# Optimization experiments

Measured on AMD Instinct MI355X. Metric: run time of the kernel, lower is better.

## Reference

```python
import jax, jax.numpy as jnp
import numpy as np

N_NODES = 100000
N_EDGES = 1600000


def setup_inputs() -> dict:
    key = jax.random.key(0)
    ks = jax.random.split(key, 8)
    x = jax.random.normal(ks[0], (N_NODES, 100), dtype=jnp.float32)
    edge_index = jax.random.randint(ks[1], (2, N_EDGES), 0, N_NODES, dtype=jnp.int64)
    edge_weight = jax.random.uniform(ks[2], (N_EDGES,), dtype=jnp.float32)
    # params (kaiming-ish scale)
    W_conv = jax.random.normal(ks[3], (100, 32), dtype=jnp.float32) * (1.0 / np.sqrt(100))
    b_conv = jnp.zeros((32,), jnp.float32)
    W1 = jax.random.normal(ks[4], (32, 16), dtype=jnp.float32) * (1.0 / np.sqrt(32))
    b1 = jnp.zeros((16,), jnp.float32)
    W2 = jax.random.normal(ks[5], (16, 8), dtype=jnp.float32) * (1.0 / np.sqrt(16))
    b2 = jnp.zeros((8,), jnp.float32)
    W3 = jax.random.normal(ks[6], (8, 10), dtype=jnp.float32) * (1.0 / np.sqrt(8))
    b3 = jnp.zeros((10,), jnp.float32)
    return {"x": x, "edge_index": edge_index, "edge_weight": edge_weight,
            "W_conv": W_conv, "b_conv": b_conv, "W1": W1, "b1": b1,
            "W2": W2, "b2": b2, "W3": W3, "b3": b3}


def gcn_conv(x, edge_index, W, b, n_nodes):
    # PyG GCNConv: add self-loops, symmetric deg^-0.5 normalization, unit edge weights
    loop = jnp.arange(n_nodes, dtype=edge_index.dtype)
    src = jnp.concatenate([edge_index[0], loop])
    dst = jnp.concatenate([edge_index[1], loop])
    deg = jax.ops.segment_sum(jnp.ones_like(dst, dtype=x.dtype), dst,
                              num_segments=n_nodes)
    dinv = jax.lax.rsqrt(jnp.maximum(deg, 1e-12))  # deg >= 1 due to self-loops
    norm = dinv[src] * dinv[dst]                   # [E+N]
    h = x @ W                                      # [N, 32]
    msg = h[src] * norm[:, None]                   # gather + scale
    out = jax.ops.segment_sum(msg, dst, num_segments=n_nodes)  # scatter-add
    return out + b


def reference(x, edge_index, edge_weight, W_conv, b_conv, W1, b1, W2, b2, W3, b3):
    # edge_weight is accepted by the original forward but never used (conv1(x, edge_index))
    n_nodes = x.shape[0]
    h = jax.nn.relu(gcn_conv(x, edge_index, W_conv, b_conv, n_nodes))
    # F.dropout with training=False (eval) is identity
    h = jax.nn.relu(h @ W1 + b1)
    h = jax.nn.relu(h @ W2 + b2)
    h = h @ W3 + b3
    return jax.nn.log_softmax(h, axis=1)
```

## Files before the change

### kernel.cpp

```cpp
#include <hip/hip_runtime.h>
#include <hip/hip_fp16.h>
#include <math.h>

#define N_NODES 100000
#define N_EDGES 1600000
#define F_IN 100
#define F_H 32

#define BKT_SHIFT 7
#define BKT_C 128
#define NBK 782
#define BKT_CAP 2560
#define BF_B 1024
#define BF_EPT 8
#define BF_TILE 8192
#define BF_GRID 196
#define AG_B 512
#define AG_CAP BKT_CAP
#define AG_EPT 5

#define XW_B 256
#define XW_R 128
#define XW_S2 51

__global__ __launch_bounds__(BF_B) void binfill_kernel(
        const int* __restrict__ src, const int* __restrict__ dst,
        int* __restrict__ gcursor, unsigned* __restrict__ packed) {
    __shared__ int cnt[NBK];
    __shared__ int lbase[NBK];
    __shared__ int gbase[NBK];
    __shared__ int wsums[16];
    __shared__ unsigned stage[BF_TILE];
    __shared__ unsigned short stageB[BF_TILE];
    __shared__ int tot;
    int t = threadIdx.x;
    long base = (long)blockIdx.x * BF_TILE;
    for (int i = t; i < NBK; i += BF_B) cnt[i] = 0;
    __syncthreads();
    int myb[BF_EPT]; int mypos[BF_EPT]; unsigned mypk[BF_EPT];
#pragma unroll
    for (int k = 0; k < BF_EPT; k++) {
        long e = base + t + (long)k * BF_B;
        myb[k] = -1;
        if (e < N_EDGES) {
            int d = dst[e];
            int sI = src[e];
            int b = d >> BKT_SHIFT;
            myb[k] = b;
            mypk[k] = (unsigned)sI | ((unsigned)(d & (BKT_C - 1)) << 17);
            mypos[k] = atomicAdd(&cnt[b], 1);
        }
    }
    __syncthreads();
    if (t < NBK && cnt[t] > 0)
        gbase[t] = t * BKT_CAP + atomicAdd(&gcursor[t], cnt[t]);
    int lane = t & 63, w = t >> 6;
    int v = (t < NBK) ? cnt[t] : 0;
    int sc = v;
#pragma unroll
    for (int off = 1; off < 64; off <<= 1) {
        int x = __shfl_up(sc, off, 64);
        if (lane >= off) sc += x;
    }
    if (lane == 63) wsums[w] = sc;
    __syncthreads();
    int pre = 0;
#pragma unroll
    for (int u = 0; u < 16; u++) pre += (u < w) ? wsums[u] : 0;
    int incl = sc + pre;
    if (t < NBK) lbase[t] = incl - v;
    if (t == BF_B - 1) tot = incl;
    __syncthreads();
#pragma unroll
    for (int k = 0; k < BF_EPT; k++) {
        if (myb[k] >= 0) {
            int p = lbase[myb[k]] + mypos[k];
            stage[p] = mypk[k];
            stageB[p] = (unsigned short)myb[k];
        }
    }
    __syncthreads();
    int T = tot;
    for (int i = t; i < T; i += BF_B) {
        int b = stageB[i];
        packed[gbase[b] + (i - lbase[b])] = stage[i];
    }
}

__global__ __launch_bounds__(XW_B) void degxw_kernel(
        const int* __restrict__ blen, const unsigned* __restrict__ packed,
        const float* __restrict__ x, const float* __restrict__ W,
        float* __restrict__ dinv, __half* __restrict__ h2) {
    __shared__ __half2 xs[XW_R * XW_S2];
    __shared__ int cnt[BKT_C];
    __shared__ float sdinv[BKT_C];
    int t = threadIdx.x;
    int b = blockIdx.x;
    if (t < BKT_C) cnt[t] = 0;
    __syncthreads();
    int beg = b * BKT_CAP, end = beg + blen[b];
    for (int i = beg + t; i < end; i += XW_B)
        atomicAdd(&cnt[(packed[i] >> 17) & (BKT_C - 1)], 1);
    __syncthreads();
    int rbase = b << BKT_SHIFT;
    int rows = min(XW_R, N_NODES - rbase);
    if (t < BKT_C) {
        float dv = rsqrtf((float)cnt[t] + 1.0f);
        sdinv[t] = dv;
        if (t < rows) dinv[rbase + t] = dv;
    }
    int total = rows * F_IN;
    const float4* gx4 = (const float4*)(x + (long)rbase * F_IN);
    for (int i4 = t; i4 < (total >> 2); i4 += XW_B) {
        float4 v = gx4[i4];
        int i = i4 << 2;
        int r = i / F_IN;
        int k = i - r * F_IN;
        __half2* p = xs + r * XW_S2 + (k >> 1);
        p[0] = __floats2half2_rn(v.x, v.y);
        p[1] = __floats2half2_rn(v.z, v.w);
    }
    __syncthreads();
    int r = t & (XW_R - 1);
    int colh16 = __builtin_amdgcn_readfirstlane((t >> 7) << 4);
    if (r < rows) {
        const float* Wp = W + colh16;
        float acc[16];
#pragma unroll
        for (int j = 0; j < 16; j++) acc[j] = 0.f;
        const __half2* xr = xs + r * XW_S2;
#pragma unroll 5
        for (int k2 = 0; k2 < F_IN / 2; k2++) {
            float2 xv = __half22float2(xr[k2]);
#pragma unroll
            for (int j = 0; j < 16; j++)
                acc[j] = fmaf(xv.y, Wp[(2 * k2 + 1) * F_H + j],
                              fmaf(xv.x, Wp[(2 * k2) * F_H + j], acc[j]));
        }
        float dv = sdinv[r];
        __half2 o[8];
#pragma unroll
        for (int j = 0; j < 8; j++)
            o[j] = __halves2half2(__float2half(acc[2 * j] * dv),
                                  __float2half(acc[2 * j + 1] * dv));
        float4* dst4 = (float4*)(h2 + (long)(rbase + r) * F_H + colh16);
        dst4[0] = ((float4*)o)[0];
        dst4[1] = ((float4*)o)[1];
    }
}

__global__ __launch_bounds__(AG_B) void agg_kernel(
        const int* __restrict__ blen, const unsigned* __restrict__ packed,
        const __half* __restrict__ h2, const float* __restrict__ dinv,
        const float* __restrict__ bc,
        const float* __restrict__ W1, const float* __restrict__ b1,
        const float* __restrict__ W2, const float* __restrict__ b2,
        const float* __restrict__ W3, const float* __restrict__ b3,
        float* __restrict__ out) {
    __shared__ float accL[BKT_C * 33];
    __shared__ int esrc[AG_CAP];
    __shared__ int cnt[BKT_C];
    __shared__ int lbase[BKT_C];
    __shared__ int wsum;
    __shared__ float sbc[32], sW1[512], sb1[16], sW2[128], sb2[8], sW3[80], sb3[10];
    int t = threadIdx.x;
    if (t < 32) sbc[t] = bc[t];
    if (t < 512) sW1[t] = W1[t];
    if (t < 16) sb1[t] = b1[t];
    if (t < 128) sW2[t] = W2[t];
    if (t < 8) sb2[t] = b2[t];
    if (t < 80) sW3[t] = W3[t];
    if (t < 10) sb3[t] = b3[t];

    int b = blockIdx.x;
    int beg = b * BKT_CAP;
    int cnum = blen[b];
    if (t < BKT_C) cnt[t] = 0;
    __syncthreads();
    unsigned pk[AG_EPT]; int pos[AG_EPT];
#pragma unroll
    for (int k = 0; k < AG_EPT; k++) {
        int idx = t + k * AG_B;
        pk[k] = 0xFFFFFFFFu;
        if (idx < cnum) {
            unsigned p = packed[beg + idx];
            pk[k] = p;
            pos[k] = atomicAdd(&cnt[(p >> 17) & (BKT_C - 1)], 1);
        }
    }
    __syncthreads();
    {
        int lane = t & 63;
        int v = 0;
        if (t < BKT_C) {
            v = cnt[t];
#pragma unroll
            for (int off = 1; off < 64; off <<= 1) {
                int xx = __shfl_up(v, off, 64);
                if (lane >= off) v += xx;
            }
            if (t == 63) wsum = v;
        }
        __syncthreads();
        if (t < BKT_C) {
            if (t >= 64) v += wsum;
            lbase[t] = v;
        }
    }
    __syncthreads();
#pragma unroll
    for (int k = 0; k < AG_EPT; k++) {
        if (pk[k] != 0xFFFFFFFFu) {
            int lid = (pk[k] >> 17) & (BKT_C - 1);
            esrc[lbase[lid] - cnt[lid] + pos[k]] = (int)(pk[k] & 0x1FFFF);
        }
    }
    __syncthreads();
    {
        int g = t >> 2, l = t & 3;
        const float4* h2o = (const float4*)h2;
        int e = lbase[g] - cnt[g];
        int eend = lbase[g];
        float a0 = 0.f, a1 = 0.f, a2 = 0.f, a3 = 0.f;
        float a4 = 0.f, a5 = 0.f, a6 = 0.f, a7 = 0.f;
        for (; e + 8 <= eend; e += 8) {
            int s0 = esrc[e], s1 = esrc[e+1], s2 = esrc[e+2], s3 = esrc[e+3];
            int s4 = esrc[e+4], s5 = esrc[e+5], s6 = esrc[e+6], s7 = esrc[e+7];
            float4 q0 = h2o[s0 * 4 + l];
            float4 q1 = h2o[s1 * 4 + l];
            float4 q2 = h2o[s2 * 4 + l];
            float4 q3 = h2o[s3 * 4 + l];
            float4 q4 = h2o[s4 * 4 + l];
            float4 q5 = h2o[s5 * 4 + l];
            float4 q6 = h2o[s6 * 4 + l];
            float4 q7 = h2o[s7 * 4 + l];
#pragma unroll
            for (int u = 0; u < 8; u++) {
                float4 q = (u == 0) ? q0 : (u == 1) ? q1 : (u == 2) ? q2 :
                           (u == 3) ? q3 : (u == 4) ? q4 : (u == 5) ? q5 :
                           (u == 6) ? q6 : q7;
                const __half2* hp = (const __half2*)&q;
                float2 f0 = __half22float2(hp[0]);
                float2 f1 = __half22float2(hp[1]);
                float2 f2 = __half22float2(hp[2]);
                float2 f3 = __half22float2(hp[3]);
                a0 += f0.x; a1 += f0.y; a2 += f1.x; a3 += f1.y;
                a4 += f2.x; a5 += f2.y; a6 += f3.x; a7 += f3.y;
            }
        }
        for (; e < eend; e++) {
            float4 q = h2o[esrc[e] * 4 + l];
            const __half2* hp = (const __half2*)&q;
            float2 f0 = __half22float2(hp[0]);
            float2 f1 = __half22float2(hp[1]);
            float2 f2 = __half22float2(hp[2]);
            float2 f3 = __half22float2(hp[3]);
            a0 += f0.x; a1 += f0.y; a2 += f1.x; a3 += f1.y;
            a4 += f2.x; a5 += f2.y; a6 += f3.x; a7 += f3.y;
        }
        float* ap = accL + g * 33 + 8 * l;
        ap[0] = a0; ap[1] = a1; ap[2] = a2; ap[3] = a3;
        ap[4] = a4; ap[5] = a5; ap[6] = a6; ap[7] = a7;
    }
    __syncthreads();

    int n = (b << BKT_SHIFT) + t;
    if (t < BKT_C && n < N_NODES) {
        float dv = dinv[n];
        const __half2* h2v = (const __half2*)h2;
        float a[32];
#pragma unroll
        for (int q = 0; q < 16; q++) {
            float2 hv = __half22float2(h2v[n * 16 + q]);
            a[2*q]   = fmaxf((accL[t * 33 + 2*q]   + hv.x) * dv + sbc[2*q],   0.f);
            a[2*q+1] = fmaxf((accL[t * 33 + 2*q+1] + hv.y) * dv + sbc[2*q+1], 0.f);
        }
        float t1[16];
#pragma unroll
        for (int j = 0; j < 16; j++) {
            float s = sb1[j];
            for (int k = 0; k < 32; k++) s += a[k] * sW1[k * 16 + j];
            t1[j] = fmaxf(s, 0.f);
        }
        float t2[8];
#pragma unroll
        for (int j = 0; j < 8; j++) {
            float s = sb2[j];
            for (int k = 0; k < 16; k++) s += t1[k] * sW2[k * 8 + j];
            t2[j] = fmaxf(s, 0.f);
        }
        float t3[10];
#pragma unroll
        for (int j = 0; j < 10; j++) {
            float s = sb3[j];
            for (int k = 0; k < 8; k++) s += t2[k] * sW3[k * 10 + j];
            t3[j] = s;
        }
        float m = t3[0];
#pragma unroll
        for (int j = 1; j < 10; j++) m = fmaxf(m, t3[j]);
        float se = 0.f;
#pragma unroll
        for (int j = 0; j < 10; j++) se += expf(t3[j] - m);
        float lse = logf(se) + m;
        float* op = out + (long)n * 10;
#pragma unroll
        for (int j = 0; j < 10; j++) op[j] = t3[j] - lse;
    }
}

extern "C" void kernel_launch(void* const* d_in, const int* in_sizes, int n_in,
                              void* d_out, int out_size, void* d_ws, size_t ws_size,
                              hipStream_t stream) {
    const float* x  = (const float*)d_in[0];
    const int*   ei = (const int*)d_in[1];
    const float* Wc = (const float*)d_in[3];
    const float* bc = (const float*)d_in[4];
    const float* W1 = (const float*)d_in[5];
    const float* b1 = (const float*)d_in[6];
    const float* W2 = (const float*)d_in[7];
    const float* b2 = (const float*)d_in[8];
    const float* W3 = (const float*)d_in[9];
    const float* b3 = (const float*)d_in[10];
    float* out = (float*)d_out;

    __half*   h2      = (__half*)d_ws;
    unsigned* packed  = (unsigned*)((char*)d_ws + (long)N_NODES * F_H * 2);
    float*    dinv    = (float*)(packed + (long)NBK * BKT_CAP);
    int*      gcursor = (int*)(dinv + N_NODES);

    const int* srcp = ei;
    const int* dstp = ei + N_EDGES;

    hipMemsetAsync(gcursor, 0, NBK * sizeof(int), stream);
    binfill_kernel<<<BF_GRID, BF_B, 0, stream>>>(srcp, dstp, gcursor, packed);
    degxw_kernel<<<NBK, XW_B, 0, stream>>>(gcursor, packed, x, Wc, dinv, h2);
    agg_kernel<<<NBK, AG_B, 0, stream>>>(gcursor, packed, h2, dinv, bc, W1, b1, W2, b2,
                                         W3, b3, out);
}
```

Before: 173.4 us.

## Split each aggregation bucket across two half-blocks of 64 destination nodes

The aggregation kernel now launches two 256-thread blocks per 128-node bucket. Each block reads the whole bucket's packed edge list but keeps only the edges whose destination falls in its half, then bins, gathers and runs the MLP for 64 nodes. This doubles the grid, cuts shared memory per block and turns the two-wavefront scan into a single-wavefront scan, aiming for higher occupancy and more parallelism. In exchange every packed edge is read twice, and each thread now holds 9 edge slots, which raises register pressure.

```diff
diff --git a/kernel.cpp b/kernel.cpp
--- a/kernel.cpp
+++ b/kernel.cpp
@@ -15,9 +15,9 @@
 #define BF_EPT 8
 #define BF_TILE 8192
 #define BF_GRID 196
-#define AG_B 512
-#define AG_CAP BKT_CAP
-#define AG_EPT 5
+#define AG_B 256
+#define AG_EPT 9
+#define AG_HCAP 1280
 
 #define XW_B 256
 #define XW_R 128
@@ -157,25 +157,25 @@
         const float* __restrict__ W2, const float* __restrict__ b2,
         const float* __restrict__ W3, const float* __restrict__ b3,
         float* __restrict__ out) {
-    __shared__ float accL[BKT_C * 33];
-    __shared__ int esrc[AG_CAP];
-    __shared__ int cnt[BKT_C];
-    __shared__ int lbase[BKT_C];
-    __shared__ int wsum;
+    __shared__ float accL[64 * 33];
+    __shared__ int esrc[AG_HCAP];
+    __shared__ int cnt[64];
+    __shared__ int lbase[64];
     __shared__ float sbc[32], sW1[512], sb1[16], sW2[128], sb2[8], sW3[80], sb3[10];
     int t = threadIdx.x;
     if (t < 32) sbc[t] = bc[t];
-    if (t < 512) sW1[t] = W1[t];
+    for (int i = t; i < 512; i += AG_B) sW1[i] = W1[i];
     if (t < 16) sb1[t] = b1[t];
     if (t < 128) sW2[t] = W2[t];
     if (t < 8) sb2[t] = b2[t];
     if (t < 80) sW3[t] = W3[t];
     if (t < 10) sb3[t] = b3[t];
 
-    int b = blockIdx.x;
-    int beg = b * BKT_CAP;
-    int cnum = blen[b];
-    if (t < BKT_C) cnt[t] = 0;
+    int bb = blockIdx.x >> 1;
+    int hh = blockIdx.x & 1;
+    int beg = bb * BKT_CAP;
+    int cnum = blen[bb];
+    if (t < 64) cnt[t] = 0;
     __syncthreads();
     unsigned pk[AG_EPT]; int pos[AG_EPT];
 #pragma unroll
@@ -184,35 +184,30 @@
         pk[k] = 0xFFFFFFFFu;
         if (idx < cnum) {
             unsigned p = packed[beg + idx];
-            pk[k] = p;
-            pos[k] = atomicAdd(&cnt[(p >> 17) & (BKT_C - 1)], 1);
-        }
-    }
-    __syncthreads();
-    {
-        int lane = t & 63;
-        int v = 0;
-        if (t < BKT_C) {
-            v = cnt[t];
-#pragma unroll
-            for (int off = 1; off < 64; off <<= 1) {
-                int xx = __shfl_up(v, off, 64);
-                if (lane >= off) v += xx;
+            int lid7 = (p >> 17) & (BKT_C - 1);
+            if ((lid7 >> 6) == hh) {
+                pk[k] = p;
+                pos[k] = atomicAdd(&cnt[lid7 & 63], 1);
             }
-            if (t == 63) wsum = v;
-        }
-        __syncthreads();
-        if (t < BKT_C) {
-            if (t >= 64) v += wsum;
-            lbase[t] = v;
-        }
+        }
+    }
+    __syncthreads();
+    if (t < 64) {
+        int v = cnt[t];
+        int sc = v;
+#pragma unroll
+        for (int off = 1; off < 64; off <<= 1) {
+            int xx = __shfl_up(sc, off, 64);
+            if ((t & 63) >= off) sc += xx;
+        }
+        lbase[t] = sc;
     }
     __syncthreads();
 #pragma unroll
     for (int k = 0; k < AG_EPT; k++) {
         if (pk[k] != 0xFFFFFFFFu) {
-            int lid = (pk[k] >> 17) & (BKT_C - 1);
-            esrc[lbase[lid] - cnt[lid] + pos[k]] = (int)(pk[k] & 0x1FFFF);
+            int g = (pk[k] >> 17) & 63;
+            esrc[lbase[g] - cnt[g] + pos[k]] = (int)(pk[k] & 0x1FFFF);
         }
     }
     __syncthreads();
@@ -264,8 +259,8 @@
     }
     __syncthreads();
 
-    int n = (b << BKT_SHIFT) + t;
-    if (t < BKT_C && n < N_NODES) {
+    int n = (bb << BKT_SHIFT) + (hh << 6) + t;
+    if (t < 64 && n < N_NODES) {
         float dv = dinv[n];
         const __half2* h2v = (const __half2*)h2;
         float a[32];
@@ -335,6 +330,6 @@
     hipMemsetAsync(gcursor, 0, NBK * sizeof(int), stream);
     binfill_kernel<<<BF_GRID, BF_B, 0, stream>>>(srcp, dstp, gcursor, packed);
     degxw_kernel<<<NBK, XW_B, 0, stream>>>(gcursor, packed, x, Wc, dinv, h2);
-    agg_kernel<<<NBK, AG_B, 0, stream>>>(gcursor, packed, h2, dinv, bc, W1, b1, W2, b2,
-                                         W3, b3, out);
+    agg_kernel<<<NBK * 2, AG_B, 0, stream>>>(gcursor, packed, h2, dinv, bc, W1, b1,
+                                             W2, b2, W3, b3, out);
 }
```

Measured after the change: 192.6 us. 1.11x slower.
